# Kernel optimization log

Measured on AMD Instinct MI355X. Metric: run time of the kernel, lower is better.

Reference implementation:

```python
import jax, jax.numpy as jnp
import numpy as np

B, LI, LT = 1, 2048, 256
H, NH, HD, MLP = 1024, 16, 64, 4096
L = LI + LT


def _make_pe():
    pos = jnp.arange(L, dtype=jnp.float32)[:, None]
    omega = 1.0 / (10000.0 ** (jnp.arange(0, HD, 2, dtype=jnp.float32) / HD))  # [HD/2]
    ang = pos * omega[None, :]                                                 # [L, HD/2]
    cos, sin = jnp.cos(ang), jnp.sin(ang)
    rot = jnp.stack([jnp.stack([cos, -sin], -1), jnp.stack([sin, cos], -1)], -2)  # [L, HD/2, 2, 2]
    return rot[None, None].astype(jnp.float32)                                 # [1,1,L,HD/2,2,2]


def setup_inputs() -> dict:
    key = jax.random.key(0)
    ks = jax.random.split(key, 20)
    w = lambda k, s: jax.random.normal(k, s, jnp.float32) * 0.02
    return {
        'img': jax.random.normal(ks[0], (B, LI, H), jnp.float32),
        'txt': jax.random.normal(ks[1], (B, LT, H), jnp.float32),
        'pe': _make_pe(),
        'vec': jax.random.normal(ks[2], (B, H), jnp.float32),
        'img_mod_w': w(ks[3], (H, 6 * H)), 'img_mod_b': w(ks[4], (6 * H,)),
        'txt_mod_w': w(ks[5], (H, 6 * H)), 'txt_mod_b': w(ks[6], (6 * H,)),
        'img_qkv_w': w(ks[7], (H, 3 * H)), 'img_qkv_b': w(ks[8], (3 * H,)),
        'img_q_scale': jnp.ones((HD,), jnp.float32), 'img_k_scale': jnp.ones((HD,), jnp.float32),
        'img_proj_w': w(ks[9], (H, H)), 'img_proj_b': w(ks[10], (H,)),
        'txt_qkv_w': w(ks[11], (H, 3 * H)), 'txt_qkv_b': w(ks[12], (3 * H,)),
        'txt_q_scale': jnp.ones((HD,), jnp.float32), 'txt_k_scale': jnp.ones((HD,), jnp.float32),
        'mlp_w1': w(ks[13], (H, MLP)), 'mlp_b1': w(ks[14], (MLP,)),
        'mlp_w2': w(ks[15], (MLP, H)), 'mlp_b2': w(ks[16], (H,)),
    }


def _ln(x):  # LayerNorm, no affine, eps=1e-6
    m = jnp.mean(x, -1, keepdims=True)
    v = jnp.mean((x - m) ** 2, -1, keepdims=True)
    return (x - m) * jax.lax.rsqrt(v + 1e-6)


def _rms(x, scale):  # QKNorm RMSNorm, eps=1e-6, learned per-dim scale
    return x * jax.lax.rsqrt(jnp.mean(x * x, -1, keepdims=True) + 1e-6) * scale


def _qkv_heads(x, w, b):
    b_, l_, _ = x.shape
    qkv = (jnp.einsum('bld,de->ble', x, w) + b).reshape(b_, l_, 3, NH, HD)
    qkv = jnp.transpose(qkv, (2, 0, 3, 1, 4))  # [3,B,H,L,D]
    return qkv[0], qkv[1], qkv[2]


def _rope(x, pe):
    xr = x.reshape(x.shape[:-1] + (HD // 2, 1, 2))  # [B,H,L,HD/2,1,2]
    out = pe[..., 0] * xr[..., 0] + pe[..., 1] * xr[..., 1]
    return out.reshape(x.shape)


def reference(img, txt, pe, vec, img_mod_w, img_mod_b, txt_mod_w, txt_mod_b,
              img_qkv_w, img_qkv_b, img_q_scale, img_k_scale, img_proj_w, img_proj_b,
              txt_qkv_w, txt_qkv_b, txt_q_scale, txt_k_scale,
              mlp_w1, mlp_b1, mlp_w2, mlp_b2):
    sv = jax.nn.silu(vec)
    imod = (jnp.einsum('bd,de->be', sv, img_mod_w) + img_mod_b)[:, None, :]
    i_shift1, i_scale1, i_gate1, i_shift2, i_scale2, i_gate2 = jnp.split(imod, 6, -1)
    tmod = (jnp.einsum('bd,de->be', sv, txt_mod_w) + txt_mod_b)[:, None, :]
    t_shift1, t_scale1 = jnp.split(tmod, 6, -1)[0], jnp.split(tmod, 6, -1)[1]

    img_m = (1 + i_scale1) * _ln(img) + i_shift1
    iq, ik, iv = _qkv_heads(img_m, img_qkv_w, img_qkv_b)
    iq, ik = _rms(iq, img_q_scale), _rms(ik, img_k_scale)

    txt_m = (1 + t_scale1) * _ln(txt) + t_shift1
    tq, tk, tv = _qkv_heads(txt_m, txt_qkv_w, txt_qkv_b)
    tq, tk = _rms(tq, txt_q_scale), _rms(tk, txt_k_scale)

    q = _rope(jnp.concatenate([tq, iq], 2), pe)
    k = _rope(jnp.concatenate([tk, ik], 2), pe)
    v = jnp.concatenate([tv, iv], 2)

    scores = jnp.einsum('bhqd,bhkd->bhqk', q, k) / np.float32(np.sqrt(HD))
    attn = jnp.einsum('bhqk,bhkd->bhqd', jax.nn.softmax(scores, -1), v)
    attn = jnp.transpose(attn, (0, 2, 1, 3)).reshape(attn.shape[0], L, NH * HD)

    img_attn = attn[:, txt.shape[1]:]
    img = img + i_gate1 * (jnp.einsum('bld,de->ble', img_attn, img_proj_w) + img_proj_b)
    h = (1 + i_scale2) * _ln(img) + i_shift2
    h = jax.nn.gelu(jnp.einsum('bld,de->ble', h, mlp_w1) + mlp_b1, approximate=True)
    h = jnp.einsum('bld,de->ble', h, mlp_w2) + mlp_b2
    return img + i_gate2 * h
```

## Files before the change

### kernel.cpp

```cpp
#include <hip/hip_runtime.h>
#include <cstdint>
#include <cstddef>

typedef unsigned short u16;
typedef __attribute__((ext_vector_type(8))) short bf16x8;
typedef __attribute__((ext_vector_type(4))) float f32x4;

#define AS1 __attribute__((address_space(1)))
#define AS3 __attribute__((address_space(3)))
#define GLDS16(g, s) __builtin_amdgcn_global_load_lds((const AS1 void*)(g), (AS3 void*)(s), 16, 0, 0)

__device__ inline u16 f2bf(float f) {
  union { float f; unsigned u; } c; c.f = f;
  unsigned r = c.u + 0x7fffu + ((c.u >> 16) & 1u);
  return (u16)(r >> 16);
}
__device__ inline float bf2f(u16 s) {
  union { unsigned u; float f; } c; c.u = ((unsigned)s) << 16;
  return c.f;
}

__global__ __launch_bounds__(256)
void wconv_t(const float* __restrict__ W, u16* __restrict__ Wt, int K, int N) {
  __shared__ float tile[32][33];
  const int tx = threadIdx.x, ty = threadIdx.y;
  const int n0 = blockIdx.x * 32, k0 = blockIdx.y * 32;
#pragma unroll
  for (int i = 0; i < 4; ++i)
    tile[ty + i * 8][tx] = W[(size_t)(k0 + ty + i * 8) * N + n0 + tx];
  __syncthreads();
#pragma unroll
  for (int i = 0; i < 4; ++i)
    Wt[(size_t)(n0 + ty + i * 8) * K + k0 + tx] = f2bf(tile[tx][ty + i * 8]);
}

__global__ __launch_bounds__(256)
void silu_kernel(const float* __restrict__ vec, float* __restrict__ sv) {
  int i = blockIdx.x * 256 + threadIdx.x;
  float x = vec[i];
  sv[i] = x / (1.f + __expf(-x));
}

__global__ __launch_bounds__(256)
void modinit(const float* __restrict__ imb, const float* __restrict__ tmb, float* __restrict__ mod) {
  int i = blockIdx.x * 256 + threadIdx.x;
  mod[i] = (i < 6144) ? imb[i] : tmb[i - 6144];
}

__global__ __launch_bounds__(256)
void modgemv(const float* __restrict__ sv, const float* __restrict__ imw,
             const float* __restrict__ tmw, float* __restrict__ mod) {
  __shared__ float s[128];
  const int t = threadIdx.x;
  const int c = blockIdx.x * 256 + t;
  const int kc = blockIdx.y * 128;
  if (t < 128) s[t] = sv[kc + t];
  __syncthreads();
  const float* W; int col;
  if (c < 6144) { W = imw; col = c; } else { W = tmw; col = c - 6144; }
  float acc = 0.f;
#pragma unroll 8
  for (int k = 0; k < 128; ++k) acc += s[k] * W[(size_t)(kc + k) * 6144 + col];
  atomicAdd(&mod[c], acc);
}

__global__ __launch_bounds__(256)
void ln_mod(const float* __restrict__ x, const float* __restrict__ shift,
            const float* __restrict__ scale, u16* __restrict__ out) {
  const int row = blockIdx.x, t = threadIdx.x;
  const float* xr = x + (size_t)row * 1024;
  float v[4], s = 0.f, sq = 0.f;
#pragma unroll
  for (int i = 0; i < 4; ++i) { v[i] = xr[t + i * 256]; s += v[i]; sq += v[i] * v[i]; }
#pragma unroll
  for (int o = 32; o; o >>= 1) { s += __shfl_down(s, o); sq += __shfl_down(sq, o); }
  __shared__ float ls[8];
  if ((t & 63) == 0) { ls[t >> 6] = s; ls[4 + (t >> 6)] = sq; }
  __syncthreads();
  s = ls[0] + ls[1] + ls[2] + ls[3];
  sq = ls[4] + ls[5] + ls[6] + ls[7];
  const float mean = s * (1.f / 1024.f);
  const float var = sq * (1.f / 1024.f) - mean * mean;
  const float rstd = rsqrtf(var + 1e-6f);
#pragma unroll
  for (int i = 0; i < 4; ++i) {
    int c = t + i * 256;
    float xn = (v[i] - mean) * rstd;
    out[(size_t)row * 1024 + c] = f2bf((1.f + scale[c]) * xn + shift[c]);
  }
}

template <int EPI, int BN>
__global__ __launch_bounds__(256, 3)
void gemm_bt(const u16* __restrict__ A, const u16* __restrict__ Bt,
             int M, int N, int K,
             const float* __restrict__ bias, const float* __restrict__ gate,
             const float* __restrict__ resid, void* __restrict__ Cout) {
  constexpr int NF = BN / 32;
  __shared__ u16 smA[128 * 32];
  __shared__ u16 smB[BN * 32];
  const int t = threadIdx.x;
  const int w = t >> 6, l = t & 63;
  const int lr = l & 15, lg = l >> 4;
  const int m0 = blockIdx.x * 128, n0 = blockIdx.y * BN;
  const int wm = (w >> 1) * 64, wn = (w & 1) * (BN / 2);
  f32x4 acc[4][NF] = {};
  const int c0 = w * 64 + l, c1 = c0 + 256;
  const int r0 = c0 >> 2, cb0 = (c0 & 3) << 3;
  const int r1 = c1 >> 2, cb1 = (c1 & 3) << 3;
  const int nk = K >> 5;
  for (int kt = 0; kt < nk; ++kt) {
    const int k0 = kt << 5;
    GLDS16(A + (size_t)(m0 + r0) * K + k0 + cb0, smA + (w * 64) * 8);
    GLDS16(A + (size_t)(m0 + r1) * K + k0 + cb1, smA + (256 + w * 64) * 8);
    GLDS16(Bt + (size_t)(n0 + r0) * K + k0 + cb0, smB + (w * 64) * 8);
    if constexpr (BN == 128)
      GLDS16(Bt + (size_t)(n0 + r1) * K + k0 + cb1, smB + (256 + w * 64) * 8);
    __syncthreads();
    bf16x8 af[4], bfr[NF];
#pragma unroll
    for (int m = 0; m < 4; ++m)
      af[m] = *(const bf16x8*)(smA + (wm + m * 16 + lr) * 32 + lg * 8);
#pragma unroll
    for (int n = 0; n < NF; ++n)
      bfr[n] = *(const bf16x8*)(smB + (wn + n * 16 + lr) * 32 + lg * 8);
#pragma unroll
    for (int m = 0; m < 4; ++m)
#pragma unroll
      for (int n = 0; n < NF; ++n)
        acc[m][n] = __builtin_amdgcn_mfma_f32_16x16x32_bf16(af[m], bfr[n], acc[m][n], 0, 0, 0);
    __syncthreads();
  }
#pragma unroll
  for (int m = 0; m < 4; ++m) {
    const int row = m0 + wm + m * 16 + lg * 4;
#pragma unroll
    for (int n = 0; n < NF; ++n) {
      const int col = n0 + wn + n * 16 + lr;
#pragma unroll
      for (int i = 0; i < 4; ++i) {
        float v = acc[m][n][i];
        size_t idx = (size_t)(row + i) * N + col;
        if constexpr (EPI == 0) {
          ((u16*)Cout)[idx] = f2bf(v + bias[col]);
        } else if constexpr (EPI == 2) {
          float cc = v + bias[col];
          float u = 0.7978845608f * (cc + 0.044715f * cc * cc * cc);
          float e = __expf(2.f * u);
          float th = 1.f - 2.f / (e + 1.f);
          ((u16*)Cout)[idx] = f2bf(0.5f * cc * (1.f + th));
        } else {
          ((float*)Cout)[idx] = resid[idx] + gate[col] * (v + bias[col]);
        }
      }
    }
  }
}

__global__ __launch_bounds__(256)
void qk_post(const u16* __restrict__ qkv_txt, const u16* __restrict__ qkv_img,
             const float* __restrict__ pe,
             const float* __restrict__ iq_s, const float* __restrict__ ik_s,
             const float* __restrict__ tq_s, const float* __restrict__ tk_s,
             u16* __restrict__ Q, u16* __restrict__ K) {
  const int d = threadIdx.x;
  const int pos = blockIdx.x * 4 + threadIdx.y;
  const int h = blockIdx.y;
  const u16* src; int r; const float *qs, *ks;
  if (pos < 256) { src = qkv_txt; r = pos; qs = tq_s; ks = tk_s; }
  else           { src = qkv_img; r = pos - 256; qs = iq_s; ks = ik_s; }
  float q = bf2f(src[(size_t)r * 3072 + h * 64 + d]);
  float k = bf2f(src[(size_t)r * 3072 + 1024 + h * 64 + d]);
  float qsq = q * q, ksq = k * k;
#pragma unroll
  for (int o = 32; o; o >>= 1) { qsq += __shfl_xor(qsq, o); ksq += __shfl_xor(ksq, o); }
  q *= rsqrtf(qsq * (1.f / 64.f) + 1e-6f) * qs[d];
  k *= rsqrtf(ksq * (1.f / 64.f) + 1e-6f) * ks[d];
  const int p = d >> 1, odd = d & 1;
  const float* pp = pe + (((size_t)pos * 32 + p) * 2 + odd) * 2;
  float qp = __shfl_xor(q, 1), kp = __shfl_xor(k, 1);
  float qe = odd ? qp : q, qo = odd ? q : qp;
  float ke = odd ? kp : k, ko = odd ? k : kp;
  float rq = pp[0] * qe + pp[1] * qo;
  float rk = pp[0] * ke + pp[1] * ko;
  size_t oidx = ((size_t)h * 2304 + pos) * 64 + d;
  Q[oidx] = f2bf(rq);
  K[oidx] = f2bf(rk);
}

__global__ __launch_bounds__(512)
void v_transpose(const u16* __restrict__ qkv_txt, const u16* __restrict__ qkv_img,
                 u16* __restrict__ Vt) {
  __shared__ float tile[64][65];
  const int tx = threadIdx.x, ty = threadIdx.y;
  const int p0 = blockIdx.x * 64, h = blockIdx.y;
#pragma unroll
  for (int i = 0; i < 8; ++i) {
    int pos = p0 + ty + i * 8;
    const u16* src; int r;
    if (pos < 256) { src = qkv_txt; r = pos; } else { src = qkv_img; r = pos - 256; }
    tile[ty + i * 8][tx] = bf2f(src[(size_t)r * 3072 + 2048 + h * 64 + tx]);
  }
  __syncthreads();
#pragma unroll
  for (int i = 0; i < 8; ++i) {
    int d = ty + i * 8;
    Vt[((size_t)h * 64 + d) * 2304 + p0 + tx] = f2bf(tile[tx][d]);
  }
}

__global__ __launch_bounds__(256, 3)
void attn_kernel(const u16* __restrict__ Q, const u16* __restrict__ Kb,
                 const u16* __restrict__ Vt, u16* __restrict__ outb) {
  __shared__ u16 smK[2][64 * 64];
  __shared__ u16 smV[2][64 * 64];
  __shared__ u16 smP[4 * 16 * 72];
  const int t = threadIdx.x, w = t >> 6, l = t & 63;
  const int lr = l & 15, lg = l >> 4;
  const int qt = blockIdx.x, h = blockIdx.y;
  const u16* Qp = Q + ((size_t)h * 2304 + qt * 64 + w * 16 + lr) * 64;
  const bf16x8 qf0 = *(const bf16x8*)(Qp + lg * 8);
  const bf16x8 qf1 = *(const bf16x8*)(Qp + 32 + lg * 8);
  const u16* Kbase = Kb + (size_t)h * 2304 * 64;
  const u16* Vbase = Vt + (size_t)h * 64 * 2304;
  f32x4 accO[4] = {};
  float mrow[4] = {-1e30f, -1e30f, -1e30f, -1e30f};
  float lrow[4] = {};
  u16* myP = smP + w * (16 * 72);

  const int c0 = w * 64 + l, c1 = c0 + 256;
  const int kr0 = c0 >> 3, ks0 = ((c0 & 7) ^ (kr0 & 7)) * 8;
  const int kr1 = c1 >> 3, ks1 = ((c1 & 7) ^ (kr1 & 7)) * 8;

  auto stage = [&](int j, int b) {
    const u16* gK = Kbase + (size_t)j * 64 * 64;
    GLDS16(gK + (size_t)kr0 * 64 + ks0, smK[b] + (w * 64) * 8);
    GLDS16(gK + (size_t)kr1 * 64 + ks1, smK[b] + (256 + w * 64) * 8);
    GLDS16(Vbase + (size_t)kr0 * 2304 + j * 64 + ks0, smV[b] + (w * 64) * 8);
    GLDS16(Vbase + (size_t)kr1 * 2304 + j * 64 + ks1, smV[b] + (256 + w * 64) * 8);
  };

  stage(0, 0);
  for (int j = 0; j < 36; ++j) {
    const int b = j & 1;
    if (j < 35) {
      stage(j + 1, b ^ 1);
      asm volatile("s_waitcnt vmcnt(4)" ::: "memory");
    } else {
      asm volatile("s_waitcnt vmcnt(0)" ::: "memory");
    }
    __builtin_amdgcn_s_barrier();
    asm volatile("" ::: "memory");

    f32x4 sf[4];
#pragma unroll
    for (int n = 0; n < 4; ++n) {
      const int row = n * 16 + lr, sw = row & 7;
      bf16x8 kf0 = *(const bf16x8*)(smK[b] + row * 64 + ((lg ^ sw) << 3));
      bf16x8 kf1 = *(const bf16x8*)(smK[b] + row * 64 + (((lg + 4) ^ sw) << 3));
      f32x4 z = {};
      z = __builtin_amdgcn_mfma_f32_16x16x32_bf16(qf0, kf0, z, 0, 0, 0);
      z = __builtin_amdgcn_mfma_f32_16x16x32_bf16(qf1, kf1, z, 0, 0, 0);
      sf[n] = z * 0.125f;
    }
    float corr[4];
#pragma unroll
    for (int i = 0; i < 4; ++i) {
      float mx = fmaxf(fmaxf(sf[0][i], sf[1][i]), fmaxf(sf[2][i], sf[3][i]));
#pragma unroll
      for (int o = 1; o < 16; o <<= 1) mx = fmaxf(mx, __shfl_xor(mx, o));
      float mnew = fmaxf(mrow[i], mx);
      corr[i] = __expf(mrow[i] - mnew);
      float rs = 0.f;
#pragma unroll
      for (int n = 0; n < 4; ++n) {
        float p = __expf(sf[n][i] - mnew);
        sf[n][i] = p;
        rs += p;
      }
#pragma unroll
      for (int o = 1; o < 16; o <<= 1) rs += __shfl_xor(rs, o);
      lrow[i] = lrow[i] * corr[i] + rs;
      mrow[i] = mnew;
    }
#pragma unroll
    for (int n = 0; n < 4; ++n)
#pragma unroll
      for (int i = 0; i < 4; ++i) {
        accO[n][i] *= corr[i];
        myP[(lg * 4 + i) * 72 + n * 16 + lr] = f2bf(sf[n][i]);
      }
#pragma unroll
    for (int c = 0; c < 2; ++c) {
      bf16x8 pf = *(const bf16x8*)(myP + lr * 72 + c * 32 + lg * 8);
#pragma unroll
      for (int nd = 0; nd < 4; ++nd) {
        const int row = nd * 16 + lr, sw = row & 7;
        bf16x8 vf = *(const bf16x8*)(smV[b] + row * 64 + (((c * 4 + lg) ^ sw) << 3));
        accO[nd] = __builtin_amdgcn_mfma_f32_16x16x32_bf16(pf, vf, accO[nd], 0, 0, 0);
      }
    }
    asm volatile("" ::: "memory");
    __builtin_amdgcn_s_barrier();
  }
#pragma unroll
  for (int nd = 0; nd < 4; ++nd) {
    const int col = h * 64 + nd * 16 + lr;
#pragma unroll
    for (int i = 0; i < 4; ++i) {
      int row = qt * 64 + w * 16 + lg * 4 + i;
      outb[(size_t)row * 1024 + col] = f2bf(accO[nd][i] / lrow[i]);
    }
  }
}

extern "C" void kernel_launch(void* const* d_in, const int* in_sizes, int n_in,
                              void* d_out, int out_size, void* d_ws, size_t ws_size,
                              hipStream_t stream) {
  const float* img         = (const float*)d_in[0];
  const float* txt         = (const float*)d_in[1];
  const float* pe          = (const float*)d_in[2];
  const float* vec         = (const float*)d_in[3];
  const float* img_mod_w   = (const float*)d_in[4];
  const float* img_mod_b   = (const float*)d_in[5];
  const float* txt_mod_w   = (const float*)d_in[6];
  const float* txt_mod_b   = (const float*)d_in[7];
  const float* img_qkv_w   = (const float*)d_in[8];
  const float* img_qkv_b   = (const float*)d_in[9];
  const float* img_q_scale = (const float*)d_in[10];
  const float* img_k_scale = (const float*)d_in[11];
  const float* img_proj_w  = (const float*)d_in[12];
  const float* img_proj_b  = (const float*)d_in[13];
  const float* txt_qkv_w   = (const float*)d_in[14];
  const float* txt_qkv_b   = (const float*)d_in[15];
  const float* txt_q_scale = (const float*)d_in[16];
  const float* txt_k_scale = (const float*)d_in[17];
  const float* mlp_w1      = (const float*)d_in[18];
  const float* mlp_b1      = (const float*)d_in[19];
  const float* mlp_w2      = (const float*)d_in[20];
  const float* mlp_b2      = (const float*)d_in[21];
  (void)in_sizes; (void)n_in; (void)out_size; (void)ws_size;

  char* ws = (char*)d_ws;
  size_t off = 0;
  auto alloc = [&](size_t bytes) -> void* {
    void* p = ws + off;
    off += (bytes + 255) & ~(size_t)255;
    return p;
  };
  float* sv     = (float*)alloc(1024 * 4);
  float* mod    = (float*)alloc(8192 * 4);
  u16* img_m    = (u16*)alloc((size_t)2048 * 1024 * 2);
  u16* txt_m    = (u16*)alloc((size_t)256 * 1024 * 2);
  u16* wt_iqkv  = (u16*)alloc((size_t)3072 * 1024 * 2);
  u16* wt_tqkv  = (u16*)alloc((size_t)3072 * 1024 * 2);
  u16* wt_proj  = (u16*)alloc((size_t)1024 * 1024 * 2);
  u16* wt_m1    = (u16*)alloc((size_t)4096 * 1024 * 2);
  u16* wt_m2    = (u16*)alloc((size_t)1024 * 4096 * 2);
  u16* qkv_img  = (u16*)alloc((size_t)2048 * 3072 * 2);
  u16* qkv_txt  = (u16*)alloc((size_t)256 * 3072 * 2);
  u16* Qb       = (u16*)alloc((size_t)16 * 2304 * 64 * 2);
  u16* Kb       = (u16*)alloc((size_t)16 * 2304 * 64 * 2);
  u16* Vtb      = (u16*)alloc((size_t)16 * 64 * 2304 * 2);
  u16* attnb    = (u16*)alloc((size_t)2304 * 1024 * 2);
  float* img2   = (float*)alloc((size_t)2048 * 1024 * 4);
  u16* h_in     = (u16*)alloc((size_t)2048 * 1024 * 2);
  u16* h1       = (u16*)alloc((size_t)2048 * 4096 * 2);

  const dim3 bT(32, 8);
  wconv_t<<<dim3(3072 / 32, 1024 / 32), bT, 0, stream>>>(img_qkv_w, wt_iqkv, 1024, 3072);
  wconv_t<<<dim3(3072 / 32, 1024 / 32), bT, 0, stream>>>(txt_qkv_w, wt_tqkv, 1024, 3072);
  wconv_t<<<dim3(1024 / 32, 1024 / 32), bT, 0, stream>>>(img_proj_w, wt_proj, 1024, 1024);
  wconv_t<<<dim3(4096 / 32, 1024 / 32), bT, 0, stream>>>(mlp_w1, wt_m1, 1024, 4096);
  wconv_t<<<dim3(1024 / 32, 4096 / 32), bT, 0, stream>>>(mlp_w2, wt_m2, 4096, 1024);

  silu_kernel<<<4, 256, 0, stream>>>(vec, sv);
  modinit<<<32, 256, 0, stream>>>(img_mod_b, txt_mod_b, mod);
  modgemv<<<dim3(32, 8), 256, 0, stream>>>(sv, img_mod_w, txt_mod_w, mod);

  ln_mod<<<2048, 256, 0, stream>>>(img, mod + 0, mod + 1024, img_m);
  ln_mod<<<256, 256, 0, stream>>>(txt, mod + 6144, mod + 7168, txt_m);

  gemm_bt<0, 128><<<dim3(16, 24), 256, 0, stream>>>(img_m, wt_iqkv, 2048, 3072, 1024,
                                                    img_qkv_b, nullptr, nullptr, qkv_img);
  gemm_bt<0, 128><<<dim3(2, 24), 256, 0, stream>>>(txt_m, wt_tqkv, 256, 3072, 1024,
                                                   txt_qkv_b, nullptr, nullptr, qkv_txt);

  qk_post<<<dim3(576, 16), dim3(64, 4), 0, stream>>>(qkv_txt, qkv_img, pe,
                                                     img_q_scale, img_k_scale,
                                                     txt_q_scale, txt_k_scale, Qb, Kb);
  v_transpose<<<dim3(36, 16), dim3(64, 8), 0, stream>>>(qkv_txt, qkv_img, Vtb);

  attn_kernel<<<dim3(36, 16), 256, 0, stream>>>(Qb, Kb, Vtb, attnb);

  gemm_bt<1, 64><<<dim3(16, 16), 256, 0, stream>>>(attnb + (size_t)256 * 1024, wt_proj,
                                                   2048, 1024, 1024,
                                                   img_proj_b, mod + 2048, img, img2);
  ln_mod<<<2048, 256, 0, stream>>>(img2, mod + 3072, mod + 4096, h_in);
  gemm_bt<2, 128><<<dim3(16, 32), 256, 0, stream>>>(h_in, wt_m1, 2048, 4096, 1024,
                                                    mlp_b1, nullptr, nullptr, h1);
  gemm_bt<3, 64><<<dim3(16, 16), 256, 0, stream>>>(h1, wt_m2, 2048, 1024, 4096,
                                                   mlp_b2, mod + 5120, img2, (float*)d_out);
}
```

Baseline: 472.2 us.

## Split attention over key range with combine pass and transposed score layout

Result: faster. 442.5 us (-6.3%).

```diff
diff --git a/kernel.cpp b/kernel.cpp
--- a/kernel.cpp
+++ b/kernel.cpp
@@ -18,6 +18,11 @@
 __device__ inline float bf2f(u16 s) {
   union { unsigned u; float f; } c; c.u = ((unsigned)s) << 16;
   return c.f;
+}
+__device__ inline unsigned cvt_pk_bf16(float a, float b) {
+  unsigned r;
+  asm("v_cvt_pk_bf16_f32 %0, %1, %2" : "=v"(r) : "v"(a), "v"(b));
+  return r;
 }
 
 __global__ __launch_bounds__(256)
@@ -184,7 +189,7 @@
   float rq = pp[0] * qe + pp[1] * qo;
   float rk = pp[0] * ke + pp[1] * ko;
   size_t oidx = ((size_t)h * 2304 + pos) * 64 + d;
-  Q[oidx] = f2bf(rq);
+  Q[oidx] = f2bf(rq * 0.125f);
   K[oidx] = f2bf(rk);
 }
 
@@ -211,21 +216,22 @@
 
 __global__ __launch_bounds__(256, 3)
 void attn_kernel(const u16* __restrict__ Q, const u16* __restrict__ Kb,
-                 const u16* __restrict__ Vt, u16* __restrict__ outb) {
+                 const u16* __restrict__ Vt,
+                 float* __restrict__ Opart, float* __restrict__ ml) {
   __shared__ u16 smK[2][64 * 64];
   __shared__ u16 smV[2][64 * 64];
   __shared__ u16 smP[4 * 16 * 72];
   const int t = threadIdx.x, w = t >> 6, l = t & 63;
   const int lr = l & 15, lg = l >> 4;
-  const int qt = blockIdx.x, h = blockIdx.y;
+  const int qt = blockIdx.x, h = blockIdx.y, sp = blockIdx.z;
+  const int j0 = sp * 18;
   const u16* Qp = Q + ((size_t)h * 2304 + qt * 64 + w * 16 + lr) * 64;
   const bf16x8 qf0 = *(const bf16x8*)(Qp + lg * 8);
   const bf16x8 qf1 = *(const bf16x8*)(Qp + 32 + lg * 8);
   const u16* Kbase = Kb + (size_t)h * 2304 * 64;
   const u16* Vbase = Vt + (size_t)h * 64 * 2304;
   f32x4 accO[4] = {};
-  float mrow[4] = {-1e30f, -1e30f, -1e30f, -1e30f};
-  float lrow[4] = {};
+  float mrun = -1e30f, lrun = 0.f;
   u16* myP = smP + w * (16 * 72);
 
   const int c0 = w * 64 + l, c1 = c0 + 256;
@@ -240,11 +246,11 @@
     GLDS16(Vbase + (size_t)kr1 * 2304 + j * 64 + ks1, smV[b] + (256 + w * 64) * 8);
   };
 
-  stage(0, 0);
-  for (int j = 0; j < 36; ++j) {
-    const int b = j & 1;
-    if (j < 35) {
-      stage(j + 1, b ^ 1);
+  stage(j0, 0);
+  for (int jj = 0; jj < 18; ++jj) {
+    const int b = jj & 1;
+    if (jj < 17) {
+      stage(j0 + jj + 1, b ^ 1);
       asm volatile("s_waitcnt vmcnt(4)" ::: "memory");
     } else {
       asm volatile("s_waitcnt vmcnt(0)" ::: "memory");
@@ -253,43 +259,63 @@
     asm volatile("" ::: "memory");
 
     f32x4 sf[4];
+    __builtin_amdgcn_s_setprio(1);
 #pragma unroll
     for (int n = 0; n < 4; ++n) {
       const int row = n * 16 + lr, sw = row & 7;
       bf16x8 kf0 = *(const bf16x8*)(smK[b] + row * 64 + ((lg ^ sw) << 3));
       bf16x8 kf1 = *(const bf16x8*)(smK[b] + row * 64 + (((lg + 4) ^ sw) << 3));
       f32x4 z = {};
-      z = __builtin_amdgcn_mfma_f32_16x16x32_bf16(qf0, kf0, z, 0, 0, 0);
-      z = __builtin_amdgcn_mfma_f32_16x16x32_bf16(qf1, kf1, z, 0, 0, 0);
-      sf[n] = z * 0.125f;
-    }
-    float corr[4];
-#pragma unroll
-    for (int i = 0; i < 4; ++i) {
-      float mx = fmaxf(fmaxf(sf[0][i], sf[1][i]), fmaxf(sf[2][i], sf[3][i]));
-#pragma unroll
-      for (int o = 1; o < 16; o <<= 1) mx = fmaxf(mx, __shfl_xor(mx, o));
-      float mnew = fmaxf(mrow[i], mx);
-      corr[i] = __expf(mrow[i] - mnew);
-      float rs = 0.f;
-#pragma unroll
-      for (int n = 0; n < 4; ++n) {
-        float p = __expf(sf[n][i] - mnew);
-        sf[n][i] = p;
-        rs += p;
-      }
-#pragma unroll
-      for (int o = 1; o < 16; o <<= 1) rs += __shfl_xor(rs, o);
-      lrow[i] = lrow[i] * corr[i] + rs;
-      mrow[i] = mnew;
-    }
-#pragma unroll
-    for (int n = 0; n < 4; ++n)
-#pragma unroll
-      for (int i = 0; i < 4; ++i) {
-        accO[n][i] *= corr[i];
-        myP[(lg * 4 + i) * 72 + n * 16 + lr] = f2bf(sf[n][i]);
-      }
+      z = __builtin_amdgcn_mfma_f32_16x16x32_bf16(kf0, qf0, z, 0, 0, 0);
+      z = __builtin_amdgcn_mfma_f32_16x16x32_bf16(kf1, qf1, z, 0, 0, 0);
+      sf[n] = z;
+    }
+    __builtin_amdgcn_s_setprio(0);
+
+    float t0 = fmaxf(fmaxf(sf[0][0], sf[0][1]), fmaxf(sf[0][2], sf[0][3]));
+    float t1 = fmaxf(fmaxf(sf[1][0], sf[1][1]), fmaxf(sf[1][2], sf[1][3]));
+    float t2 = fmaxf(fmaxf(sf[2][0], sf[2][1]), fmaxf(sf[2][2], sf[2][3]));
+    float t3 = fmaxf(fmaxf(sf[3][0], sf[3][1]), fmaxf(sf[3][2], sf[3][3]));
+    float mx = fmaxf(fmaxf(t0, t1), fmaxf(t2, t3));
+    mx = fmaxf(mx, __shfl_xor(mx, 16));
+    mx = fmaxf(mx, __shfl_xor(mx, 32));
+    const float mnew = fmaxf(mrun, mx);
+    const float corr = __expf(mrun - mnew);
+    mrun = mnew;
+
+    float p[4][4];
+    float s0 = 0.f, s1 = 0.f, s2 = 0.f, s3 = 0.f;
+#pragma unroll
+    for (int n = 0; n < 4; ++n) {
+      p[n][0] = __expf(sf[n][0] - mnew);
+      p[n][1] = __expf(sf[n][1] - mnew);
+      p[n][2] = __expf(sf[n][2] - mnew);
+      p[n][3] = __expf(sf[n][3] - mnew);
+    }
+    s0 = (p[0][0] + p[0][1]) + (p[0][2] + p[0][3]);
+    s1 = (p[1][0] + p[1][1]) + (p[1][2] + p[1][3]);
+    s2 = (p[2][0] + p[2][1]) + (p[2][2] + p[2][3]);
+    s3 = (p[3][0] + p[3][1]) + (p[3][2] + p[3][3]);
+    float rs = (s0 + s1) + (s2 + s3);
+    rs += __shfl_xor(rs, 16);
+    rs += __shfl_xor(rs, 32);
+    lrun = lrun * corr + rs;
+
+#pragma unroll
+    for (int n = 0; n < 4; ++n) {
+      *(unsigned*)(myP + lr * 72 + n * 16 + lg * 4)     = cvt_pk_bf16(p[n][0], p[n][1]);
+      *(unsigned*)(myP + lr * 72 + n * 16 + lg * 4 + 2) = cvt_pk_bf16(p[n][2], p[n][3]);
+    }
+
+    float cb[4];
+#pragma unroll
+    for (int i = 0; i < 4; ++i) cb[i] = __shfl(corr, lg * 4 + i);
+#pragma unroll
+    for (int nd = 0; nd < 4; ++nd)
+#pragma unroll
+      for (int i = 0; i < 4; ++i) accO[nd][i] *= cb[i];
+
+    __builtin_amdgcn_s_setprio(1);
 #pragma unroll
     for (int c = 0; c < 2; ++c) {
       bf16x8 pf = *(const bf16x8*)(myP + lr * 72 + c * 32 + lg * 8);
@@ -300,18 +326,40 @@
         accO[nd] = __builtin_amdgcn_mfma_f32_16x16x32_bf16(pf, vf, accO[nd], 0, 0, 0);
       }
     }
+    __builtin_amdgcn_s_setprio(0);
     asm volatile("" ::: "memory");
     __builtin_amdgcn_s_barrier();
   }
-#pragma unroll
-  for (int nd = 0; nd < 4; ++nd) {
-    const int col = h * 64 + nd * 16 + lr;
-#pragma unroll
-    for (int i = 0; i < 4; ++i) {
-      int row = qt * 64 + w * 16 + lg * 4 + i;
-      outb[(size_t)row * 1024 + col] = f2bf(accO[nd][i] / lrow[i]);
-    }
-  }
+
+  float* Op = Opart + (((size_t)(sp * 16 + h) * 2304) + qt * 64) * 64;
+#pragma unroll
+  for (int nd = 0; nd < 4; ++nd)
+#pragma unroll
+    for (int i = 0; i < 4; ++i)
+      Op[(size_t)(w * 16 + lg * 4 + i) * 64 + nd * 16 + lr] = accO[nd][i];
+  if (lg == 0) {
+    size_t mi = ((size_t)(sp * 16 + h) * 2304 + qt * 64 + w * 16 + lr) * 2;
+    ml[mi] = mrun;
+    ml[mi + 1] = lrun;
+  }
+}
+
+__global__ __launch_bounds__(256)
+void attn_combine(const float* __restrict__ Opart, const float* __restrict__ ml,
+                  u16* __restrict__ outb) {
+  int idx = blockIdx.x * 256 + threadIdx.x;
+  int q = idx >> 10, c = idx & 1023;
+  int h = c >> 6, d = c & 63;
+  size_t i0 = (size_t)h * 2304 + q;
+  size_t i1 = (size_t)(16 + h) * 2304 + q;
+  float m0 = ml[i0 * 2], l0 = ml[i0 * 2 + 1];
+  float m1 = ml[i1 * 2], l1 = ml[i1 * 2 + 1];
+  float M = fmaxf(m0, m1);
+  float w0 = __expf(m0 - M), w1 = __expf(m1 - M);
+  float a0 = Opart[i0 * 64 + d], a1 = Opart[i1 * 64 + d];
+  float num = w0 * a0 + w1 * a1;
+  float den = w0 * l0 + w1 * l1;
+  outb[(size_t)q * 1024 + c] = f2bf(num / den);
 }
 
 extern "C" void kernel_launch(void* const* d_in, const int* in_sizes, int n_in,
@@ -350,15 +398,17 @@
   };
   float* sv     = (float*)alloc(1024 * 4);
   float* mod    = (float*)alloc(8192 * 4);
+  u16* qkv_img  = (u16*)alloc((size_t)2048 * 3072 * 2);
+  u16* qkv_txt  = (u16*)alloc((size_t)256 * 3072 * 2);
   u16* img_m    = (u16*)alloc((size_t)2048 * 1024 * 2);
   u16* txt_m    = (u16*)alloc((size_t)256 * 1024 * 2);
+  float* Opart  = (float*)qkv_img;
+  float* mlbuf  = (float*)alloc((size_t)2 * 16 * 2304 * 2 * 4);
   u16* wt_iqkv  = (u16*)alloc((size_t)3072 * 1024 * 2);
   u16* wt_tqkv  = (u16*)alloc((size_t)3072 * 1024 * 2);
   u16* wt_proj  = (u16*)alloc((size_t)1024 * 1024 * 2);
   u16* wt_m1    = (u16*)alloc((size_t)4096 * 1024 * 2);
   u16* wt_m2    = (u16*)alloc((size_t)1024 * 4096 * 2);
-  u16* qkv_img  = (u16*)alloc((size_t)2048 * 3072 * 2);
-  u16* qkv_txt  = (u16*)alloc((size_t)256 * 3072 * 2);
   u16* Qb       = (u16*)alloc((size_t)16 * 2304 * 64 * 2);
   u16* Kb       = (u16*)alloc((size_t)16 * 2304 * 64 * 2);
   u16* Vtb      = (u16*)alloc((size_t)16 * 64 * 2304 * 2);
@@ -391,7 +441,8 @@
                                                      txt_q_scale, txt_k_scale, Qb, Kb);
   v_transpose<<<dim3(36, 16), dim3(64, 8), 0, stream>>>(qkv_txt, qkv_img, Vtb);
 
-  attn_kernel<<<dim3(36, 16), 256, 0, stream>>>(Qb, Kb, Vtb, attnb);
+  attn_kernel<<<dim3(36, 16, 2), 256, 0, stream>>>(Qb, Kb, Vtb, Opart, mlbuf);
+  attn_combine<<<9216, 256, 0, stream>>>(Opart, mlbuf, attnb);
 
   gemm_bt<1, 64><<<dim3(16, 16), 256, 0, stream>>>(attnb + (size_t)256 * 1024, wt_proj,
                                                    2048, 1024, 1024,
```
